# Performance work log

Measured on AMD Instinct MI355X. Metric: run time of the kernel, lower is better.

The kernel has to match this reference:

```python
import jax, jax.numpy as jnp
import numpy as np

B, C, H, W = 8, 256, 128, 128
RED = 4
LAMBDA_C = 0.5
LAMBDA_S = 0.5
EPS = 1e-5  # BatchNorm eps (eval mode: running stats)


def setup_inputs() -> dict:
    key = jax.random.key(0)
    ks = jax.random.split(key, 8)
    Cr = C // RED
    x1 = jax.random.normal(ks[0], (B, C, H, W), jnp.float32)
    x2 = jax.random.normal(ks[1], (B, C, H, W), jnp.float32)
    # feature_extractor: 1x1 conv (dim*2 -> dim), kaiming-ish scale
    w_fe = jax.random.normal(ks[2], (C, 2 * C), jnp.float32) * (2.0 / (2 * C)) ** 0.5
    bn_gamma = jnp.ones((C,), jnp.float32)
    bn_beta = jnp.zeros((C,), jnp.float32)
    bn_mean = jnp.zeros((C,), jnp.float32)
    bn_var = jnp.ones((C,), jnp.float32)
    # conv_weight_generator: C -> C//r -> 9C (1x1 convs on pooled vector)
    w_cg1 = jax.random.normal(ks[3], (Cr, C), jnp.float32) * (2.0 / C) ** 0.5
    w_cg2 = jax.random.normal(ks[4], (9 * C, Cr), jnp.float32) * (2.0 / Cr) ** 0.5
    # attention_generator: C -> C//r -> 2
    w_ag1 = jax.random.normal(ks[5], (Cr, C), jnp.float32) * (2.0 / C) ** 0.5
    w_ag2 = jax.random.normal(ks[6], (2, Cr), jnp.float32) * (2.0 / Cr) ** 0.5
    return {"x1": x1, "x2": x2, "w_fe": w_fe, "bn_gamma": bn_gamma,
            "bn_beta": bn_beta, "bn_mean": bn_mean, "bn_var": bn_var,
            "w_cg1": w_cg1, "w_cg2": w_cg2, "w_ag1": w_ag1, "w_ag2": w_ag2}


def reference(x1, x2, w_fe, bn_gamma, bn_beta, bn_mean, bn_var,
              w_cg1, w_cg2, w_ag1, w_ag2):
    Bv, Cv, Hv, Wv = x1.shape
    # feature_extractor: 1x1 conv + BN (eval) + ReLU
    cat = jnp.concatenate([x1, x2], axis=1)                       # [B,2C,H,W]
    s = jnp.einsum('oi,bihw->bohw', w_fe, cat)                    # [B,C,H,W]
    scale = (bn_gamma / jnp.sqrt(bn_var + EPS))[None, :, None, None]
    shift = (bn_beta - bn_mean * bn_gamma / jnp.sqrt(bn_var + EPS))[None, :, None, None]
    s = jax.nn.relu(s * scale + shift)
    # global average pool -> per-sample vectors
    pooled = s.mean(axis=(2, 3))                                  # [B,C]
    # dynamic per-sample, per-channel 3x3 kernels
    hcg = jax.nn.relu(pooled @ w_cg1.T)                           # [B,C//r]
    cw = (hcg @ w_cg2.T).reshape(Bv * Cv, 1, 3, 3)                # [B*C,1,3,3]
    # attention scalars (2 per sample)
    attn = jax.nn.sigmoid(jax.nn.relu(pooled @ w_ag1.T) @ w_ag2.T)  # [B,2]

    def dyn_conv(x):
        xr = x.reshape(1, Bv * Cv, Hv, Wv)
        y = jax.lax.conv_general_dilated(
            xr, cw, window_strides=(1, 1), padding='SAME',
            feature_group_count=Bv * Cv,
            dimension_numbers=('NCHW', 'OIHW', 'NCHW'))
        return y.reshape(Bv, Cv, Hv, Wv)

    d1 = dyn_conv(x1)
    d2 = dyn_conv(x2)
    a1 = attn[:, 0][:, None, None, None]
    a2 = attn[:, 1][:, None, None, None]
    out_x1 = x1 + LAMBDA_C * a1 * d1
    out_x2 = x2 + LAMBDA_C * a2 * d2
    return LAMBDA_S * out_x1 + (1.0 - LAMBDA_S) * out_x2
```

## Files before the change

kernel.cpp:

```cpp
#include <hip/hip_runtime.h>
#include <stdint.h>
#include <math.h>

#define HW_ 16384
#define C_  256
#define NT  8

typedef long i64;
typedef float f32x4 __attribute__((ext_vector_type(4)));
typedef long i64x2 __attribute__((ext_vector_type(2)));
typedef unsigned int u32;

__global__ __launch_bounds__(256) void k0_prep(
    const float* __restrict__ w_fe, const float* __restrict__ gamma,
    const float* __restrict__ beta, const float* __restrict__ mean,
    const float* __restrict__ var, u32* __restrict__ Wp,
    float* __restrict__ scale, float* __restrict__ shift)
{
  int i = blockIdx.x * 256 + threadIdx.x;
  if (i < 32768) {
    int e0  = (i & 1) * 4;
    int r15 = (i >> 1) & 15;
    int kg  = (i >> 5) & 3;
    int mf  = (i >> 7) & 15;
    int ks  = i >> 11;
    int row = mf * 16 + r15;
    int k   = ks * 32 + kg * 8 + e0;
    const float* src = w_fe + row * 512 + k;
    u32 w = 0;
    w = __builtin_amdgcn_cvt_pk_fp8_f32(src[0], src[1], w, false);
    w = __builtin_amdgcn_cvt_pk_fp8_f32(src[2], src[3], w, true);
    Wp[i] = w;
  }
  if (i < 256) {
    float sc = gamma[i] * rsqrtf(var[i] + 1e-5f);
    scale[i] = sc;
    shift[i] = beta[i] - mean[i] * sc;
  }
}

__global__ __launch_bounds__(1024, 4) void k1_gemm_pool(
    const float* __restrict__ x1, const float* __restrict__ x2,
    const u32* __restrict__ Wp,
    const float* __restrict__ scale, const float* __restrict__ shift,
    float* __restrict__ pool_part)
{
  __shared__ __align__(16) char Bl[2][32768];

  const int tid  = threadIdx.x;
  const int wave = tid >> 6;
  const int lane = tid & 63;
  const int r15  = lane & 15;
  const int kg   = lane >> 4;
  const int blk  = blockIdx.x;
  const int b    = blk >> 5;
  const int tile0 = (blk & 31) * NT;

  const float* xb1 = x1 + (size_t)b * C_ * HW_;
  const float* xb2 = x2 + (size_t)b * C_ * HW_;

  const int p2  = tid & 31;
  const int k8  = tid >> 5;
  const int ksL = k8 >> 2;
  const int kgs = k8 & 3;
  const int nfs = p2 >> 3;
  const int L0  = ((2 * p2) & 15) + kgs * 16;
  const int WB0 = (ksL * 2 + (nfs >> 1)) * 1024 + L0 * 16 + (nfs & 1) * 8;

  i64 Af[16];
#pragma unroll
  for (int ks = 0; ks < 16; ++ks)
    Af[ks] = *(const i64*)((const char*)Wp
             + ((ks * 16 + wave) * 64 + kg * 16 + r15) * 8);

  const int chbase = wave * 16 + kg * 4;
  const float4 sc4 = *(const float4*)&scale[chbase];
  const float4 sh4 = *(const float4*)&shift[chbase];

  float pool0 = 0.f, pool1 = 0.f, pool2 = 0.f, pool3 = 0.f;

  float2 gR[8];

#define ISSUE_H(H, P0)                                                        \
  {                                                                           \
    const float* s0 = ((H) == 0 ? xb1 : xb2) + (size_t)(k8 * 8) * HW_         \
                      + (P0) + 2 * p2;                                        \
    _Pragma("unroll")                                                         \
    for (int r = 0; r < 8; ++r) gR[r] = *(const float2*)(s0 + r * HW_);       \
  }

#define WRITE_H(H, BUF)                                                       \
  {                                                                           \
    u32 a0 = 0, a1 = 0, b0 = 0, b1 = 0;                                       \
    a0 = __builtin_amdgcn_cvt_pk_fp8_f32(gR[0].x, gR[1].x, a0, false);        \
    a0 = __builtin_amdgcn_cvt_pk_fp8_f32(gR[2].x, gR[3].x, a0, true);         \
    a1 = __builtin_amdgcn_cvt_pk_fp8_f32(gR[4].x, gR[5].x, a1, false);        \
    a1 = __builtin_amdgcn_cvt_pk_fp8_f32(gR[6].x, gR[7].x, a1, true);         \
    b0 = __builtin_amdgcn_cvt_pk_fp8_f32(gR[0].y, gR[1].y, b0, false);        \
    b0 = __builtin_amdgcn_cvt_pk_fp8_f32(gR[2].y, gR[3].y, b0, true);         \
    b1 = __builtin_amdgcn_cvt_pk_fp8_f32(gR[4].y, gR[5].y, b1, false);        \
    b1 = __builtin_amdgcn_cvt_pk_fp8_f32(gR[6].y, gR[7].y, b1, true);         \
    char* wb = (char*)(BUF) + WB0 + (H) * 16384;                              \
    u32* w0 = (u32*)(wb);                                                     \
    w0[0] = a0; w0[1] = a1;                                    \
    u32* w1 = (u32*)(wb + 16);                                                \
    w1[0] = b0; w1[1] = b1;                                    \
  }

#define COMPUTE_H(H, BUF)                                                     \
  {                                                                           \
    _Pragma("unroll")                                                         \
    for (int ks8 = 0; ks8 < 8; ++ks8) {                                       \
      const int ks = (H) * 8 + ks8;                                           \
      const char* rbase = (const char*)(BUF) + ks * 2048 + lane * 16;         \
      _Pragma("unroll")                                                       \
      for (int np = 0; np < 2; ++np) {                                        \
        i64x2 bq = *(const i64x2*)(rbase + np * 1024);                        \
        acc[np * 2] = __builtin_amdgcn_mfma_f32_16x16x32_fp8_fp8(             \
            Af[ks], bq.x, acc[np * 2], 0, 0, 0);                              \
        acc[np * 2 + 1] = __builtin_amdgcn_mfma_f32_16x16x32_fp8_fp8(         \
            Af[ks], bq.y, acc[np * 2 + 1], 0, 0, 0);                          \
      }                                                                       \
    }                                                                         \
  }

  ISSUE_H(0, tile0 * 64) WRITE_H(0, Bl[0])
  ISSUE_H(1, tile0 * 64) WRITE_H(1, Bl[0])
  __syncthreads();

  for (int tt = 0; tt < NT; ++tt) {
    f32x4 acc[4];
#pragma unroll
    for (int nf = 0; nf < 4; ++nf) acc[nf] = (f32x4){0.f, 0.f, 0.f, 0.f};

    const int p0n = (tile0 + tt + 1) * 64;
    const bool more = (tt + 1 < NT);
    const char* cb = Bl[tt & 1];
    char* nxt = Bl[(tt + 1) & 1];

    if (more) ISSUE_H(0, p0n)
    COMPUTE_H(0, cb)
    if (more) { WRITE_H(0, nxt) ISSUE_H(1, p0n) }
    COMPUTE_H(1, cb)
    if (more) WRITE_H(1, nxt)

#pragma unroll
    for (int nf = 0; nf < 4; ++nf) {
      pool0 += fmaxf(acc[nf][0] * sc4.x + sh4.x, 0.f);
      pool1 += fmaxf(acc[nf][1] * sc4.y + sh4.y, 0.f);
      pool2 += fmaxf(acc[nf][2] * sc4.z + sh4.z, 0.f);
      pool3 += fmaxf(acc[nf][3] * sc4.w + sh4.w, 0.f);
    }
    __syncthreads();
  }

#pragma unroll
  for (int m = 1; m < 16; m <<= 1) {
    pool0 += __shfl_xor(pool0, m);
    pool1 += __shfl_xor(pool1, m);
    pool2 += __shfl_xor(pool2, m);
    pool3 += __shfl_xor(pool3, m);
  }
  if (r15 == 0) {
    float* dst = pool_part + (size_t)blk * 256 + chbase;
    dst[0] = pool0; dst[1] = pool1; dst[2] = pool2; dst[3] = pool3;
  }
}

__global__ __launch_bounds__(256) void k2_small(
    const float* __restrict__ pool_part,
    const float* __restrict__ w_cg1, const float* __restrict__ w_cg2,
    const float* __restrict__ w_ag1, const float* __restrict__ w_ag2,
    float* __restrict__ cw, float* __restrict__ coef)
{
  __shared__ float pl[256];
  __shared__ float hl[64];
  const int bi = blockIdx.x;
  const int b = bi / 10, j = bi % 10;
  const int t = threadIdx.x;
  float s = 0.f;
  const float* base = pool_part + (size_t)b * 32 * 256 + t;
  for (int blk = 0; blk < 32; ++blk) s += base[blk * 256];
  pl[t] = s * (1.0f / 16384.0f);
  __syncthreads();
  if (j < 9) {
    if (t < 64) {
      float h = 0.f;
      for (int i = 0; i < 256; ++i) h += pl[i] * w_cg1[t * 256 + i];
      hl[t] = fmaxf(h, 0.f);
    }
    __syncthreads();
    const int o = t * 9 + j;
    float acc = 0.f;
    for (int jj = 0; jj < 64; ++jj) acc += hl[jj] * w_cg2[o * 64 + jj];
    cw[b * 2304 + o] = acc;
  } else {
    if (t < 64) {
      float a = 0.f;
      for (int i = 0; i < 256; ++i) a += pl[i] * w_ag1[t * 256 + i];
      hl[t] = fmaxf(a, 0.f);
    }
    __syncthreads();
    if (t < 2) {
      float acc = 0.f;
      for (int jj = 0; jj < 64; ++jj) acc += hl[jj] * w_ag2[t * 64 + jj];
      coef[b * 2 + t] = 0.25f / (1.0f + expf(-acc));
    }
  }
}

__global__ __launch_bounds__(256) void k3_dynconv(
    const float* __restrict__ x1, const float* __restrict__ x2,
    const float* __restrict__ cw, const float* __restrict__ coef,
    float* __restrict__ out)
{
  __shared__ float t1[34 * 128];
  __shared__ float t2[34 * 128];
  const int tid   = threadIdx.x;
  const int blk   = blockIdx.x;
  const int strip = blk & 3;
  const int c     = (blk >> 2) & 255;
  const int b     = blk >> 10;
  const int h0    = strip * 32;

  const size_t plane = ((size_t)b * C_ + c) * HW_;
  const float* p1 = x1 + plane;
  const float* p2 = x2 + plane;

  float tp[9];
#pragma unroll
  for (int e = 0; e < 9; ++e) tp[e] = cw[(b * C_ + c) * 9 + e];
  const float c1 = coef[b * 2 + 0];
  const float c2 = coef[b * 2 + 1];

  for (int f = tid; f < 1088; f += 256) {
    int row = f >> 5;
    int c4  = (f & 31) << 2;
    int gh  = h0 - 1 + row;
    float4 v1 = make_float4(0.f, 0.f, 0.f, 0.f), v2 = v1;
    if (gh >= 0 && gh < 128) {
      v1 = *(const float4*)&p1[gh * 128 + c4];
      v2 = *(const float4*)&p2[gh * 128 + c4];
    }
    *(float4*)&t1[row * 128 + c4] = v1;
    *(float4*)&t2[row * 128 + c4] = v2;
  }
  __syncthreads();

  for (int i = 0; i < 16; ++i) {
    int q   = tid + i * 256;
    int r   = q >> 7;
    int col = q & 127;
    int lr  = r + 1;
    const bool lok = col > 0, rok = col < 127;
    float d1 = 0.f, d2 = 0.f;
#pragma unroll
    for (int dy = 0; dy < 3; ++dy) {
      const float* row1 = &t1[(lr - 1 + dy) * 128];
      const float* row2 = &t2[(lr - 1 + dy) * 128];
      float a1v = lok ? row1[col - 1] : 0.f;
      float b1v = row1[col];
      float e1v = rok ? row1[col + 1] : 0.f;
      float a2v = lok ? row2[col - 1] : 0.f;
      float b2v = row2[col];
      float e2v = rok ? row2[col + 1] : 0.f;
      d1 += a1v * tp[dy * 3 + 0] + b1v * tp[dy * 3 + 1] + e1v * tp[dy * 3 + 2];
      d2 += a2v * tp[dy * 3 + 0] + b2v * tp[dy * 3 + 1] + e2v * tp[dy * 3 + 2];
    }
    float v1 = t1[lr * 128 + col];
    float v2 = t2[lr * 128 + col];
    out[plane + (size_t)(h0 + r) * 128 + col] = 0.5f * (v1 + v2) + c1 * d1 + c2 * d2;
  }
}

extern "C" void kernel_launch(void* const* d_in, const int* in_sizes, int n_in,
                              void* d_out, int out_size, void* d_ws, size_t ws_size,
                              hipStream_t stream) {
  const float* x1    = (const float*)d_in[0];
  const float* x2    = (const float*)d_in[1];
  const float* w_fe  = (const float*)d_in[2];
  const float* gamma = (const float*)d_in[3];
  const float* beta  = (const float*)d_in[4];
  const float* mean  = (const float*)d_in[5];
  const float* var   = (const float*)d_in[6];
  const float* w_cg1 = (const float*)d_in[7];
  const float* w_cg2 = (const float*)d_in[8];
  const float* w_ag1 = (const float*)d_in[9];
  const float* w_ag2 = (const float*)d_in[10];
  float* out = (float*)d_out;

  char* ws = (char*)d_ws;
  u32* Wp          = (u32*)(ws);
  float* scale     = (float*)(ws + 131072);
  float* shift     = (float*)(ws + 132096);
  float* pool_part = (float*)(ws + 133120);
  float* cw        = (float*)(ws + 395264);
  float* coef      = (float*)(ws + 468992);

  k0_prep<<<128, 256, 0, stream>>>(w_fe, gamma, beta, mean, var, Wp, scale, shift);
  k1_gemm_pool<<<256, 1024, 0, stream>>>(x1, x2, Wp, scale, shift, pool_part);
  k2_small<<<80, 256, 0, stream>>>(pool_part, w_cg1, w_cg2, w_ag1, w_ag2, cw, coef);
  k3_dynconv<<<8192, 256, 0, stream>>>(x1, x2, cw, coef, out);
}
```

Baseline: 153.1 us.

## Deepen global-load prefetch to two tiles ahead with dual register buffers

Global loads of x1/x2 now land in two register buffers (gA, gB) and are issued two tiles ahead instead of one. Each load has a full tile of MFMA work to hide behind before its fp8 conversion and LDS write. The per-tile __syncthreads is replaced by an inline s_waitcnt lgkmcnt(0) plus s_barrier, so the barrier no longer waits on outstanding global (vmem) loads. This raises register pressure, and it relies on the asm barrier alone to order the LDS writes against later reads.

```diff
diff --git a/kernel.cpp b/kernel.cpp
--- a/kernel.cpp
+++ b/kernel.cpp
@@ -10,6 +10,8 @@
 typedef float f32x4 __attribute__((ext_vector_type(4)));
 typedef long i64x2 __attribute__((ext_vector_type(2)));
 typedef unsigned int u32;
+
+#define BARRIER_LGKM() asm volatile("s_waitcnt lgkmcnt(0)\n\ts_barrier" ::: "memory")
 
 __global__ __launch_bounds__(256) void k0_prep(
     const float* __restrict__ w_fe, const float* __restrict__ gamma,
@@ -79,27 +81,27 @@
 
   float pool0 = 0.f, pool1 = 0.f, pool2 = 0.f, pool3 = 0.f;
 
-  float2 gR[8];
-
-#define ISSUE_H(H, P0)                                                        \
+  float2 gA[8], gB[8];
+
+#define ISSUE_HB(G, H, P0)                                                    \
   {                                                                           \
     const float* s0 = ((H) == 0 ? xb1 : xb2) + (size_t)(k8 * 8) * HW_         \
                       + (P0) + 2 * p2;                                        \
     _Pragma("unroll")                                                         \
-    for (int r = 0; r < 8; ++r) gR[r] = *(const float2*)(s0 + r * HW_);       \
-  }
-
-#define WRITE_H(H, BUF)                                                       \
+    for (int r = 0; r < 8; ++r) G[r] = *(const float2*)(s0 + r * HW_);        \
+  }
+
+#define WRITE_HB(G, H, BUF)                                                   \
   {                                                                           \
     u32 a0 = 0, a1 = 0, b0 = 0, b1 = 0;                                       \
-    a0 = __builtin_amdgcn_cvt_pk_fp8_f32(gR[0].x, gR[1].x, a0, false);        \
-    a0 = __builtin_amdgcn_cvt_pk_fp8_f32(gR[2].x, gR[3].x, a0, true);         \
-    a1 = __builtin_amdgcn_cvt_pk_fp8_f32(gR[4].x, gR[5].x, a1, false);        \
-    a1 = __builtin_amdgcn_cvt_pk_fp8_f32(gR[6].x, gR[7].x, a1, true);         \
-    b0 = __builtin_amdgcn_cvt_pk_fp8_f32(gR[0].y, gR[1].y, b0, false);        \
-    b0 = __builtin_amdgcn_cvt_pk_fp8_f32(gR[2].y, gR[3].y, b0, true);         \
-    b1 = __builtin_amdgcn_cvt_pk_fp8_f32(gR[4].y, gR[5].y, b1, false);        \
-    b1 = __builtin_amdgcn_cvt_pk_fp8_f32(gR[6].y, gR[7].y, b1, true);         \
+    a0 = __builtin_amdgcn_cvt_pk_fp8_f32(G[0].x, G[1].x, a0, false);          \
+    a0 = __builtin_amdgcn_cvt_pk_fp8_f32(G[2].x, G[3].x, a0, true);           \
+    a1 = __builtin_amdgcn_cvt_pk_fp8_f32(G[4].x, G[5].x, a1, false);          \
+    a1 = __builtin_amdgcn_cvt_pk_fp8_f32(G[6].x, G[7].x, a1, true);           \
+    b0 = __builtin_amdgcn_cvt_pk_fp8_f32(G[0].y, G[1].y, b0, false);          \
+    b0 = __builtin_amdgcn_cvt_pk_fp8_f32(G[2].y, G[3].y, b0, true);           \
+    b1 = __builtin_amdgcn_cvt_pk_fp8_f32(G[4].y, G[5].y, b1, false);          \
+    b1 = __builtin_amdgcn_cvt_pk_fp8_f32(G[6].y, G[7].y, b1, true);           \
     char* wb = (char*)(BUF) + WB0 + (H) * 16384;                              \
     u32* w0 = (u32*)(wb);                                                     \
     w0[0] = a0; w0[1] = a1;                                    \
@@ -124,8 +126,12 @@
     }                                                                         \
   }
 
-  ISSUE_H(0, tile0 * 64) WRITE_H(0, Bl[0])
-  ISSUE_H(1, tile0 * 64) WRITE_H(1, Bl[0])
+  ISSUE_HB(gA, 0, tile0 * 64)
+  ISSUE_HB(gB, 1, tile0 * 64)
+  WRITE_HB(gA, 0, Bl[0])
+  WRITE_HB(gB, 1, Bl[0])
+  ISSUE_HB(gA, 0, (tile0 + 1) * 64)
+  ISSUE_HB(gB, 1, (tile0 + 1) * 64)
   __syncthreads();
 
   for (int tt = 0; tt < NT; ++tt) {
@@ -133,16 +139,18 @@
 #pragma unroll
     for (int nf = 0; nf < 4; ++nf) acc[nf] = (f32x4){0.f, 0.f, 0.f, 0.f};
 
-    const int p0n = (tile0 + tt + 1) * 64;
-    const bool more = (tt + 1 < NT);
+    const int p0i = (tile0 + tt + 2) * 64;
+    const bool wri = (tt + 1 < NT);
+    const bool iss = (tt + 2 < NT);
     const char* cb = Bl[tt & 1];
     char* nxt = Bl[(tt + 1) & 1];
 
-    if (more) ISSUE_H(0, p0n)
     COMPUTE_H(0, cb)
-    if (more) { WRITE_H(0, nxt) ISSUE_H(1, p0n) }
+    if (wri) WRITE_HB(gA, 0, nxt)
+    if (iss) ISSUE_HB(gA, 0, p0i)
     COMPUTE_H(1, cb)
-    if (more) WRITE_H(1, nxt)
+    if (wri) WRITE_HB(gB, 1, nxt)
+    if (iss) ISSUE_HB(gB, 1, p0i)
 
 #pragma unroll
     for (int nf = 0; nf < 4; ++nf) {
@@ -151,7 +159,7 @@
       pool2 += fmaxf(acc[nf][2] * sc4.z + sh4.z, 0.f);
       pool3 += fmaxf(acc[nf][3] * sc4.w + sh4.w, 0.f);
     }
-    __syncthreads();
+    BARRIER_LGKM();
   }
 
 #pragma unroll
```

Measured after the change: 152.8 us. Within noise of the previous version (-0.2%).

## Double pixel tile width per iteration with float4 loads and lighter barrier

Applied to the files above, without the earlier changes.

Each loop iteration of the fused GEMM+pool kernel now covers 128 pixels instead of 64, using float4 global loads. The LDS buffers double to 128 KB total and each tile issues twice as many MFMAs, while the iteration count is halved. The per-iteration __syncthreads is replaced by an inline lgkmcnt wait plus s_barrier. The larger LDS footprint and the extra accumulators reduce how many blocks can be resident per CU, and skipping the vmcnt wait is safe only if no global-memory ordering is needed at that barrier.

```diff
diff --git a/kernel.cpp b/kernel.cpp
--- a/kernel.cpp
+++ b/kernel.cpp
@@ -4,12 +4,14 @@
 
 #define HW_ 16384
 #define C_  256
-#define NT  8
+#define NT  4
 
 typedef long i64;
 typedef float f32x4 __attribute__((ext_vector_type(4)));
 typedef long i64x2 __attribute__((ext_vector_type(2)));
 typedef unsigned int u32;
+
+#define BARRIER_LGKM() asm volatile("s_waitcnt lgkmcnt(0)\n\ts_barrier" ::: "memory")
 
 __global__ __launch_bounds__(256) void k0_prep(
     const float* __restrict__ w_fe, const float* __restrict__ gamma,
@@ -45,7 +47,7 @@
     const float* __restrict__ scale, const float* __restrict__ shift,
     float* __restrict__ pool_part)
 {
-  __shared__ __align__(16) char Bl[2][32768];
+  __shared__ __align__(16) char Bl[2][65536];
 
   const int tid  = threadIdx.x;
   const int wave = tid >> 6;
@@ -59,13 +61,12 @@
   const float* xb1 = x1 + (size_t)b * C_ * HW_;
   const float* xb2 = x2 + (size_t)b * C_ * HW_;
 
-  const int p2  = tid & 31;
-  const int k8  = tid >> 5;
-  const int ksL = k8 >> 2;
-  const int kgs = k8 & 3;
-  const int nfs = p2 >> 3;
-  const int L0  = ((2 * p2) & 15) + kgs * 16;
-  const int WB0 = (ksL * 2 + (nfs >> 1)) * 1024 + L0 * 16 + (nfs & 1) * 8;
+  const int p4  = (tid & 31) * 4;
+  const int k8p = tid >> 5;
+  const int nfs = p4 >> 4;
+  const int slot0 = (p4 & 15) + (k8p & 3) * 16;
+  const int WB0 = ((k8p >> 2) * 4 + (nfs >> 1)) * 1024 + slot0 * 16
+                  + (nfs & 1) * 8;
 
   i64 Af[16];
 #pragma unroll
@@ -79,32 +80,30 @@
 
   float pool0 = 0.f, pool1 = 0.f, pool2 = 0.f, pool3 = 0.f;
 
-  float2 gR[8];
-
-#define ISSUE_H(H, P0)                                                        \
+  float4 gS[8];
+
+#define ISSUE_HB(H, P0)                                                       \
   {                                                                           \
-    const float* s0 = ((H) == 0 ? xb1 : xb2) + (size_t)(k8 * 8) * HW_         \
-                      + (P0) + 2 * p2;                                        \
+    const float* s0 = ((H) == 0 ? xb1 : xb2) + (size_t)(k8p * 8) * HW_        \
+                      + (P0) + p4;                                            \
     _Pragma("unroll")                                                         \
-    for (int r = 0; r < 8; ++r) gR[r] = *(const float2*)(s0 + r * HW_);       \
-  }
-
-#define WRITE_H(H, BUF)                                                       \
+    for (int r = 0; r < 8; ++r) gS[r] = *(const float4*)(s0 + r * HW_);       \
+  }
+
+#define WRITE_HB(H, BUF)                                                      \
   {                                                                           \
-    u32 a0 = 0, a1 = 0, b0 = 0, b1 = 0;                                       \
-    a0 = __builtin_amdgcn_cvt_pk_fp8_f32(gR[0].x, gR[1].x, a0, false);        \
-    a0 = __builtin_amdgcn_cvt_pk_fp8_f32(gR[2].x, gR[3].x, a0, true);         \
-    a1 = __builtin_amdgcn_cvt_pk_fp8_f32(gR[4].x, gR[5].x, a1, false);        \
-    a1 = __builtin_amdgcn_cvt_pk_fp8_f32(gR[6].x, gR[7].x, a1, true);         \
-    b0 = __builtin_amdgcn_cvt_pk_fp8_f32(gR[0].y, gR[1].y, b0, false);        \
-    b0 = __builtin_amdgcn_cvt_pk_fp8_f32(gR[2].y, gR[3].y, b0, true);         \
-    b1 = __builtin_amdgcn_cvt_pk_fp8_f32(gR[4].y, gR[5].y, b1, false);        \
-    b1 = __builtin_amdgcn_cvt_pk_fp8_f32(gR[6].y, gR[7].y, b1, true);         \
-    char* wb = (char*)(BUF) + WB0 + (H) * 16384;                              \
-    u32* w0 = (u32*)(wb);                                                     \
-    w0[0] = a0; w0[1] = a1;                                    \
-    u32* w1 = (u32*)(wb + 16);                                                \
-    w1[0] = b0; w1[1] = b1;                                    \
+    char* wb0 = (char*)(BUF) + WB0 + (H) * 32768;                             \
+    _Pragma("unroll")                                                         \
+    for (int i = 0; i < 4; ++i) {                                             \
+      const float* gp = (const float*)gS;                                     \
+      u32 w0 = 0, w1 = 0;                                                     \
+      w0 = __builtin_amdgcn_cvt_pk_fp8_f32(gp[0 * 4 + i], gp[1 * 4 + i], w0, false); \
+      w0 = __builtin_amdgcn_cvt_pk_fp8_f32(gp[2 * 4 + i], gp[3 * 4 + i], w0, true);  \
+      w1 = __builtin_amdgcn_cvt_pk_fp8_f32(gp[4 * 4 + i], gp[5 * 4 + i], w1, false); \
+      w1 = __builtin_amdgcn_cvt_pk_fp8_f32(gp[6 * 4 + i], gp[7 * 4 + i], w1, true);  \
+      u32* wb = (u32*)(wb0 + i * 16);                                         \
+      wb[0] = w0; wb[1] = w1;                                                 \
+    }                                                                         \
   }
 
 #define COMPUTE_H(H, BUF)                                                     \
@@ -112,9 +111,9 @@
     _Pragma("unroll")                                                         \
     for (int ks8 = 0; ks8 < 8; ++ks8) {                                       \
       const int ks = (H) * 8 + ks8;                                           \
-      const char* rbase = (const char*)(BUF) + ks * 2048 + lane * 16;         \
+      const char* rbase = (const char*)(BUF) + ks * 4096 + lane * 16;         \
       _Pragma("unroll")                                                       \
-      for (int np = 0; np < 2; ++np) {                                        \
+      for (int np = 0; np < 4; ++np) {                                        \
         i64x2 bq = *(const i64x2*)(rbase + np * 1024);                        \
         acc[np * 2] = __builtin_amdgcn_mfma_f32_16x16x32_fp8_fp8(             \
             Af[ks], bq.x, acc[np * 2], 0, 0, 0);                              \
@@ -124,34 +123,34 @@
     }                                                                         \
   }
 
-  ISSUE_H(0, tile0 * 64) WRITE_H(0, Bl[0])
-  ISSUE_H(1, tile0 * 64) WRITE_H(1, Bl[0])
+  ISSUE_HB(0, tile0 * 128) WRITE_HB(0, Bl[0])
+  ISSUE_HB(1, tile0 * 128) WRITE_HB(1, Bl[0])
   __syncthreads();
 
   for (int tt = 0; tt < NT; ++tt) {
-    f32x4 acc[4];
-#pragma unroll
-    for (int nf = 0; nf < 4; ++nf) acc[nf] = (f32x4){0.f, 0.f, 0.f, 0.f};
-
-    const int p0n = (tile0 + tt + 1) * 64;
+    f32x4 acc[8];
+#pragma unroll
+    for (int nf = 0; nf < 8; ++nf) acc[nf] = (f32x4){0.f, 0.f, 0.f, 0.f};
+
+    const int p0n = (tile0 + tt + 1) * 128;
     const bool more = (tt + 1 < NT);
     const char* cb = Bl[tt & 1];
     char* nxt = Bl[(tt + 1) & 1];
 
-    if (more) ISSUE_H(0, p0n)
+    if (more) ISSUE_HB(0, p0n)
     COMPUTE_H(0, cb)
-    if (more) { WRITE_H(0, nxt) ISSUE_H(1, p0n) }
+    if (more) { WRITE_HB(0, nxt) ISSUE_HB(1, p0n) }
     COMPUTE_H(1, cb)
-    if (more) WRITE_H(1, nxt)
-
-#pragma unroll
-    for (int nf = 0; nf < 4; ++nf) {
+    if (more) WRITE_HB(1, nxt)
+
+#pragma unroll
+    for (int nf = 0; nf < 8; ++nf) {
       pool0 += fmaxf(acc[nf][0] * sc4.x + sh4.x, 0.f);
       pool1 += fmaxf(acc[nf][1] * sc4.y + sh4.y, 0.f);
       pool2 += fmaxf(acc[nf][2] * sc4.z + sh4.z, 0.f);
       pool3 += fmaxf(acc[nf][3] * sc4.w + sh4.w, 0.f);
     }
-    __syncthreads();
+    BARRIER_LGKM();
   }
 
 #pragma unroll
```

After: 223.0 us. +45.6%, slower.

## Pre-pack inputs to FP8 in MFMA layout and stream via global_load_lds

Applied to the files above, without the earlier changes.

Adds a separate packing kernel that converts x1/x2 to FP8 once and writes them in the exact tile layout the GEMM consumes. The GEMM kernel then streams those packed tiles directly into LDS with asynchronous global_load_lds and vmcnt-based barriers, instead of converting and scattering in registers. Each block now handles 128-pixel tiles with a larger double buffer. The aim is to cut GEMM-side conversion and LDS write overhead, but it adds an extra read of the fp32 inputs plus a 64 MB workspace write and read. The old path is kept as a fallback for when the workspace is too small.

```diff
diff --git a/kernel.cpp b/kernel.cpp
--- a/kernel.cpp
+++ b/kernel.cpp
@@ -4,12 +4,20 @@
 
 #define HW_ 16384
 #define C_  256
-#define NT  8
 
 typedef long i64;
 typedef float f32x4 __attribute__((ext_vector_type(4)));
 typedef long i64x2 __attribute__((ext_vector_type(2)));
 typedef unsigned int u32;
+
+__device__ __forceinline__ void gload_lds16(const void* g, void* l) {
+  __builtin_amdgcn_global_load_lds((const __attribute__((address_space(1))) u32*)g,
+                                   (__attribute__((address_space(3))) u32*)l, 16, 0, 0);
+}
+
+#define VMBAR4() asm volatile("s_waitcnt vmcnt(4)\n\ts_barrier" ::: "memory")
+#define VMBAR0() asm volatile("s_waitcnt vmcnt(0)\n\ts_barrier" ::: "memory")
+#define BAR()    asm volatile("s_barrier" ::: "memory")
 
 __global__ __launch_bounds__(256) void k0_prep(
     const float* __restrict__ w_fe, const float* __restrict__ gamma,
@@ -39,13 +47,62 @@
   }
 }
 
+__global__ __launch_bounds__(256) void kq_pack(
+    const float* __restrict__ x1, const float* __restrict__ x2,
+    char* __restrict__ Xq)
+{
+  __shared__ char T[8192];
+  const int tid  = threadIdx.x;
+  const int bq   = blockIdx.x;
+  const int half = bq & 1;
+  const int k8g  = (bq >> 1) & 63;
+  const int b    = bq >> 7;
+  const int H    = k8g >> 5;
+  const int ko   = k8g & 31;
+  const int fbb  = H * 32 + (ko >> 2) * 4;
+  const int kg   = ko & 3;
+
+  const float* xs = (H ? x2 : x1) + ((size_t)b * C_ + ko * 8) * HW_;
+  const int r  = tid >> 5;
+  const int pc = (tid & 31) * 4;
+
+  const int a0base = ((pc >> 5) & 3) * 256 + (pc & 15) * 16 + ((pc >> 4) & 1) * 8 + r;
+
+  for (int n = 0; n < 8; ++n) {
+    const float* s0 = xs + (size_t)r * HW_ + half * 8192 + n * 1024 + pc;
+    float4 g[8];
+#pragma unroll
+    for (int j = 0; j < 8; ++j) g[j] = *(const float4*)(s0 + j * 128);
+    __syncthreads();
+#pragma unroll
+    for (int j = 0; j < 8; ++j) {
+      u32 w0 = 0, w1 = 0;
+      w0 = __builtin_amdgcn_cvt_pk_fp8_f32(g[j].x, g[j].y, w0, false);
+      w1 = __builtin_amdgcn_cvt_pk_fp8_f32(g[j].z, g[j].w, w1, false);
+      int a0 = j * 1024 + a0base;
+      T[a0]      = (char)(w0 & 0xff);
+      T[a0 + 16] = (char)((w0 >> 8) & 0xff);
+      T[a0 + 32] = (char)(w1 & 0xff);
+      T[a0 + 48] = (char)((w1 >> 8) & 0xff);
+    }
+    __syncthreads();
+#pragma unroll
+    for (int q2 = 0; q2 < 2; ++q2) {
+      int u = tid * 16 + q2 * 4096;
+      int tloc = u >> 10, nf2 = (u >> 8) & 3, inoff = u & 255;
+      char* dst = Xq + ((size_t)(b * 128 + half * 64 + n * 8 + tloc) << 16)
+                  + (fbb + nf2) * 1024 + kg * 256 + inoff;
+      *(float4*)dst = *(const float4*)&T[u];
+    }
+  }
+}
+
 __global__ __launch_bounds__(1024, 4) void k1_gemm_pool(
-    const float* __restrict__ x1, const float* __restrict__ x2,
-    const u32* __restrict__ Wp,
+    const char* __restrict__ Xq, const u32* __restrict__ Wp,
     const float* __restrict__ scale, const float* __restrict__ shift,
     float* __restrict__ pool_part)
 {
-  __shared__ __align__(16) char Bl[2][32768];
+  __shared__ __align__(16) char Bl[2][65536];
 
   const int tid  = threadIdx.x;
   const int wave = tid >> 6;
@@ -54,11 +111,99 @@
   const int kg   = lane >> 4;
   const int blk  = blockIdx.x;
   const int b    = blk >> 5;
-  const int tile0 = (blk & 31) * NT;
-
+  const int t0   = (blk & 31) * 4;
+
+  i64 Af[16];
+#pragma unroll
+  for (int ks = 0; ks < 16; ++ks)
+    Af[ks] = *(const i64*)((const char*)Wp
+             + ((ks * 16 + wave) * 64 + kg * 16 + r15) * 8);
+
+  const int chbase = wave * 16 + kg * 4;
+  const float4 sc4 = *(const float4*)&scale[chbase];
+  const float4 sh4 = *(const float4*)&shift[chbase];
+
+  float pool0 = 0.f, pool1 = 0.f, pool2 = 0.f, pool3 = 0.f;
+
+  const int ldsw = (tid & 0xFFC0) * 16;
+
+#define GISSUE(I, BUF)                                                        \
+  {                                                                           \
+    const char* img = Xq + ((size_t)(b * 128 + t0 + (I)) << 16) + tid * 16;   \
+    _Pragma("unroll")                                                         \
+    for (int ps = 0; ps < 4; ++ps)                                            \
+      gload_lds16(img + ps * 16384, (char*)(BUF) + ps * 16384 + ldsw);        \
+  }
+
+#define COMPUTE_T(BUF)                                                        \
+  {                                                                           \
+    _Pragma("unroll")                                                         \
+    for (int ks = 0; ks < 16; ++ks) {                                         \
+      const char* rbase = (const char*)(BUF) + ks * 4096 + lane * 16;         \
+      _Pragma("unroll")                                                       \
+      for (int np = 0; np < 4; ++np) {                                        \
+        i64x2 bq2 = *(const i64x2*)(rbase + np * 1024);                       \
+        acc[np * 2] = __builtin_amdgcn_mfma_f32_16x16x32_fp8_fp8(             \
+            Af[ks], bq2.x, acc[np * 2], 0, 0, 0);                             \
+        acc[np * 2 + 1] = __builtin_amdgcn_mfma_f32_16x16x32_fp8_fp8(         \
+            Af[ks], bq2.y, acc[np * 2 + 1], 0, 0, 0);                         \
+      }                                                                       \
+    }                                                                         \
+  }
+
+  GISSUE(0, Bl[0])
+  GISSUE(1, Bl[1])
+
+#pragma unroll
+  for (int t = 0; t < 4; ++t) {
+    f32x4 acc[8];
+#pragma unroll
+    for (int nf = 0; nf < 8; ++nf) acc[nf] = (f32x4){0.f, 0.f, 0.f, 0.f};
+
+    if (t < 3) { VMBAR4(); } else { VMBAR0(); }
+    COMPUTE_T(Bl[t & 1])
+
+#pragma unroll
+    for (int nf = 0; nf < 8; ++nf) {
+      pool0 += fmaxf(acc[nf][0] * sc4.x + sh4.x, 0.f);
+      pool1 += fmaxf(acc[nf][1] * sc4.y + sh4.y, 0.f);
+      pool2 += fmaxf(acc[nf][2] * sc4.z + sh4.z, 0.f);
+      pool3 += fmaxf(acc[nf][3] * sc4.w + sh4.w, 0.f);
+    }
+    BAR();
+    if (t + 2 < 4) GISSUE(t + 2, Bl[t & 1])
+  }
+
+#pragma unroll
+  for (int m = 1; m < 16; m <<= 1) {
+    pool0 += __shfl_xor(pool0, m);
+    pool1 += __shfl_xor(pool1, m);
+    pool2 += __shfl_xor(pool2, m);
+    pool3 += __shfl_xor(pool3, m);
+  }
+  if (r15 == 0) {
+    float* dst = pool_part + (size_t)blk * 256 + chbase;
+    dst[0] = pool0; dst[1] = pool1; dst[2] = pool2; dst[3] = pool3;
+  }
+}
+
+__global__ __launch_bounds__(1024, 4) void k1_fb(
+    const float* __restrict__ x1, const float* __restrict__ x2,
+    const u32* __restrict__ Wp,
+    const float* __restrict__ scale, const float* __restrict__ shift,
+    float* __restrict__ pool_part)
+{
+  __shared__ __align__(16) char Bl[2][32768];
+  const int tid  = threadIdx.x;
+  const int wave = tid >> 6;
+  const int lane = tid & 63;
+  const int r15  = lane & 15;
+  const int kg   = lane >> 4;
+  const int blk  = blockIdx.x;
+  const int b    = blk >> 5;
+  const int tile0 = (blk & 31) * 8;
   const float* xb1 = x1 + (size_t)b * C_ * HW_;
   const float* xb2 = x2 + (size_t)b * C_ * HW_;
-
   const int p2  = tid & 31;
   const int k8  = tid >> 5;
   const int ksL = k8 >> 2;
@@ -66,32 +211,23 @@
   const int nfs = p2 >> 3;
   const int L0  = ((2 * p2) & 15) + kgs * 16;
   const int WB0 = (ksL * 2 + (nfs >> 1)) * 1024 + L0 * 16 + (nfs & 1) * 8;
-
   i64 Af[16];
 #pragma unroll
   for (int ks = 0; ks < 16; ++ks)
     Af[ks] = *(const i64*)((const char*)Wp
              + ((ks * 16 + wave) * 64 + kg * 16 + r15) * 8);
-
   const int chbase = wave * 16 + kg * 4;
   const float4 sc4 = *(const float4*)&scale[chbase];
   const float4 sh4 = *(const float4*)&shift[chbase];
-
   float pool0 = 0.f, pool1 = 0.f, pool2 = 0.f, pool3 = 0.f;
-
   float2 gR[8];
-
-#define ISSUE_H(H, P0)                                                        \
-  {                                                                           \
-    const float* s0 = ((H) == 0 ? xb1 : xb2) + (size_t)(k8 * 8) * HW_         \
+#define FISSUE(H, P0)                                                         \
+  { const float* s0 = ((H) == 0 ? xb1 : xb2) + (size_t)(k8 * 8) * HW_         \
                       + (P0) + 2 * p2;                                        \
     _Pragma("unroll")                                                         \
-    for (int r = 0; r < 8; ++r) gR[r] = *(const float2*)(s0 + r * HW_);       \
-  }
-
-#define WRITE_H(H, BUF)                                                       \
-  {                                                                           \
-    u32 a0 = 0, a1 = 0, b0 = 0, b1 = 0;                                       \
+    for (int rr = 0; rr < 8; ++rr) gR[rr] = *(const float2*)(s0 + rr * HW_); }
+#define FWRITE(H, BUF)                                                        \
+  { u32 a0 = 0, a1 = 0, b0 = 0, b1 = 0;                                       \
     a0 = __builtin_amdgcn_cvt_pk_fp8_f32(gR[0].x, gR[1].x, a0, false);        \
     a0 = __builtin_amdgcn_cvt_pk_fp8_f32(gR[2].x, gR[3].x, a0, true);         \
     a1 = __builtin_amdgcn_cvt_pk_fp8_f32(gR[4].x, gR[5].x, a1, false);        \
@@ -101,49 +237,37 @@
     b1 = __builtin_amdgcn_cvt_pk_fp8_f32(gR[4].y, gR[5].y, b1, false);        \
     b1 = __builtin_amdgcn_cvt_pk_fp8_f32(gR[6].y, gR[7].y, b1, true);         \
     char* wb = (char*)(BUF) + WB0 + (H) * 16384;                              \
-    u32* w0 = (u32*)(wb);                                                     \
-    w0[0] = a0; w0[1] = a1;                                    \
-    u32* w1 = (u32*)(wb + 16);                                                \
-    w1[0] = b0; w1[1] = b1;                                    \
-  }
-
-#define COMPUTE_H(H, BUF)                                                     \
-  {                                                                           \
-    _Pragma("unroll")                                                         \
+    u32* w0p = (u32*)(wb); w0p[0] = a0; w0p[1] = a1;                          \
+    u32* w1p = (u32*)(wb + 16); w1p[0] = b0; w1p[1] = b1; }
+#define FCOMP(H, BUF)                                                         \
+  { _Pragma("unroll")                                                         \
     for (int ks8 = 0; ks8 < 8; ++ks8) {                                       \
       const int ks = (H) * 8 + ks8;                                           \
       const char* rbase = (const char*)(BUF) + ks * 2048 + lane * 16;         \
       _Pragma("unroll")                                                       \
       for (int np = 0; np < 2; ++np) {                                        \
-        i64x2 bq = *(const i64x2*)(rbase + np * 1024);                        \
+        i64x2 bq2 = *(const i64x2*)(rbase + np * 1024);                       \
         acc[np * 2] = __builtin_amdgcn_mfma_f32_16x16x32_fp8_fp8(             \
-            Af[ks], bq.x, acc[np * 2], 0, 0, 0);                              \
+            Af[ks], bq2.x, acc[np * 2], 0, 0, 0);                             \
         acc[np * 2 + 1] = __builtin_amdgcn_mfma_f32_16x16x32_fp8_fp8(         \
-            Af[ks], bq.y, acc[np * 2 + 1], 0, 0, 0);                          \
-      }                                                                       \
-    }                                                                         \
-  }
-
-  ISSUE_H(0, tile0 * 64) WRITE_H(0, Bl[0])
-  ISSUE_H(1, tile0 * 64) WRITE_H(1, Bl[0])
+            Af[ks], bq2.y, acc[np * 2 + 1], 0, 0, 0);                         \
+      } } }
+  FISSUE(0, tile0 * 64) FWRITE(0, Bl[0])
+  FISSUE(1, tile0 * 64) FWRITE(1, Bl[0])
   __syncthreads();
-
-  for (int tt = 0; tt < NT; ++tt) {
+  for (int tt = 0; tt < 8; ++tt) {
     f32x4 acc[4];
 #pragma unroll
     for (int nf = 0; nf < 4; ++nf) acc[nf] = (f32x4){0.f, 0.f, 0.f, 0.f};
-
     const int p0n = (tile0 + tt + 1) * 64;
-    const bool more = (tt + 1 < NT);
+    const bool more = (tt + 1 < 8);
     const char* cb = Bl[tt & 1];
     char* nxt = Bl[(tt + 1) & 1];
-
-    if (more) ISSUE_H(0, p0n)
-    COMPUTE_H(0, cb)
-    if (more) { WRITE_H(0, nxt) ISSUE_H(1, p0n) }
-    COMPUTE_H(1, cb)
-    if (more) WRITE_H(1, nxt)
-
+    if (more) FISSUE(0, p0n)
+    FCOMP(0, cb)
+    if (more) { FWRITE(0, nxt) FISSUE(1, p0n) }
+    FCOMP(1, cb)
+    if (more) FWRITE(1, nxt)
 #pragma unroll
     for (int nf = 0; nf < 4; ++nf) {
       pool0 += fmaxf(acc[nf][0] * sc4.x + sh4.x, 0.f);
@@ -153,7 +277,6 @@
     }
     __syncthreads();
   }
-
 #pragma unroll
   for (int m = 1; m < 16; m <<= 1) {
     pool0 += __shfl_xor(pool0, m);
@@ -296,9 +419,16 @@
   float* pool_part = (float*)(ws + 133120);
   float* cw        = (float*)(ws + 395264);
   float* coef      = (float*)(ws + 468992);
+  char* Xq         = ws + 524288;
+  const size_t NEED = 524288 + (size_t)8 * 128 * 65536;
 
   k0_prep<<<128, 256, 0, stream>>>(w_fe, gamma, beta, mean, var, Wp, scale, shift);
-  k1_gemm_pool<<<256, 1024, 0, stream>>>(x1, x2, Wp, scale, shift, pool_part);
+  if (ws_size >= NEED) {
+    kq_pack<<<1024, 256, 0, stream>>>(x1, x2, Xq);
+    k1_gemm_pool<<<256, 1024, 0, stream>>>(Xq, Wp, scale, shift, pool_part);
+  } else {
+    k1_fb<<<256, 1024, 0, stream>>>(x1, x2, Wp, scale, shift, pool_part);
+  }
   k2_small<<<80, 256, 0, stream>>>(pool_part, w_cg1, w_cg2, w_ag1, w_ag2, cw, coef);
   k3_dynconv<<<8192, 256, 0, stream>>>(x1, x2, cw, coef, out);
 }
```

New measurement: 220.9 us. 44.3% more time.
